# Performance work log

Measured on AMD Instinct MI355X. Metric: run time of the kernel, lower is better.

The kernel has to match this reference:

```python
import jax, jax.numpy as jnp
import numpy as np

H = 256        # hidden_channels (== out_channels)
IN = 128       # in_channels (atom features)
ED = 64        # edge_dim (bond features)
G = 1024       # num graphs
L = 48         # atoms per graph (static pad length)
N = G * L      # num atoms
E = 2 * N      # num directed edges
NLAYERS = 4


def setup_inputs() -> dict:
    key = jax.random.key(0)
    ks = jax.random.split(key, 12)
    def rn(k, shape, scale=0.05):
        return jax.random.normal(k, shape, jnp.float32) * scale
    return {
        "x": jax.random.normal(ks[0], (N, IN), jnp.float32),
        "edge_attr": jax.random.normal(ks[1], (E, ED), jnp.float32),
        "edge_index": jax.random.randint(ks[2], (2, E), 0, N),
        "batch": jnp.repeat(jnp.arange(G), L),  # sorted, L atoms per graph
        "w_atom": rn(ks[3], (IN, H)), "b_atom": jnp.zeros((H,), jnp.float32),
        "w_bond": rn(ks[4], (ED, H)), "b_bond": jnp.zeros((H,), jnp.float32),
        "conv_w": rn(ks[5], (NLAYERS, H, H)), "conv_b": jnp.zeros((NLAYERS, H), jnp.float32),
        "w_lin": rn(ks[6], (3 * H, H)), "b_lin": jnp.zeros((H,), jnp.float32),
        "gru_bias": rn(ks[7], (H,), 0.06),
        "w_ih": rn(ks[8], (2, 3 * H, H)), "w_hh": rn(ks[9], (2, 3 * H, H)),
        "b_ih": jnp.zeros((2, 3 * H), jnp.float32), "b_hh": jnp.zeros((2, 3 * H), jnp.float32),
        "w_out": rn(ks[10], (2 * H, H)), "b_out": jnp.zeros((H,), jnp.float32),
    }


def reference(x, edge_attr, edge_index, batch, w_atom, b_atom, w_bond, b_bond,
              conv_w, conv_b, w_lin, b_lin, gru_bias, w_ih, w_hh, b_ih, b_hh,
              w_out, b_out):
    relu = jax.nn.relu
    row, col = edge_index[0], edge_index[1]  # flow='target_to_source': aggregate at row

    x_proj = relu(x @ w_atom + b_atom)                 # [N, H]
    h_atom = x_proj
    h_bond = relu(edge_attr @ w_bond + b_bond)         # [E, H]

    def booster(h_bond):
        # message_booster multi-aggregation: sum * max (empty slots -> 0, as torch_scatter)
        s = jax.ops.segment_sum(h_bond, row, num_segments=N)
        m = jax.ops.segment_max(h_bond, row, num_segments=N)
        m = jnp.where(jnp.isfinite(m), m, 0.0)
        return s * m

    for i in range(NLAYERS - 1):
        h_atom = h_atom + booster(h_bond)              # additive communicator
        # edge_update: x[edge_index_i] - edge_attr[edge_index_j]; seq = Linear+ReLU (dropout p=0)
        h_bond = relu((h_atom[row] - h_bond[col]) @ conv_w[i] + conv_b[i])
    aggr_message = h_atom + booster(h_bond)            # last conv; edge output discarded

    h = jnp.concatenate([aggr_message, h_atom, x_proj], axis=1) @ w_lin + b_lin  # [N, H]

    # ---- BatchGRU ----
    msg = relu(h + gru_bias)
    starts = jnp.searchsorted(batch, jnp.arange(G))
    pos = jnp.arange(N) - starts[batch]                # position within own graph
    messages = jnp.zeros((G, L, H), h.dtype).at[batch, pos].set(msg)
    h0 = jax.ops.segment_max(h, batch, num_segments=G)  # [G, H], same init both dirs

    def gru_dir(seq, d):
        def cell(hst, x_t):
            gi = x_t @ w_ih[d].T + b_ih[d]
            gh = hst @ w_hh[d].T + b_hh[d]
            i_r, i_z, i_n = jnp.split(gi, 3, -1)
            h_r, h_z, h_n = jnp.split(gh, 3, -1)
            r = jax.nn.sigmoid(i_r + h_r)
            z = jax.nn.sigmoid(i_z + h_z)
            n = jnp.tanh(i_n + r * h_n)
            hn = (1.0 - z) * n + z * hst
            return hn, hn
        _, out = jax.lax.scan(cell, h0, seq)
        return out

    seq = messages.transpose(1, 0, 2)                  # [L, G, H]
    out_f = gru_dir(seq, 0)
    out_b = gru_dir(seq[::-1], 1)[::-1]
    h_msgs = jnp.concatenate([out_f, out_b], -1).transpose(1, 0, 2)  # [G, L, 2H]
    unpadded = h_msgs[batch, pos]                      # [N, 2H]

    return relu(unpadded @ w_out + b_out)              # seq_out (dropout p=0)
```

## Files before the change

kernel.cpp:

```cpp
#include <hip/hip_runtime.h>
#include <math.h>

#define HH 256
#define GG 1024
#define LL 48
#define NNODES 49152
#define NEDGES 98304
#define SB 256.0f
#define DSB 0.00390625f

typedef _Float16 f16;
typedef __attribute__((ext_vector_type(8))) _Float16 f16x8;
typedef __attribute__((ext_vector_type(4))) float f32x4;

#define MFMA16(a, b, c) __builtin_amdgcn_mfma_f32_16x16x32_f16(a, b, c, 0, 0, 0)

__device__ inline float sc_from_max(float m) {
    if (!(m > 0.f)) return 1.0f;
    return ldexpf(1.0f, 13 - ilogbf(m));
}

__global__ void csr_count(const int* __restrict__ row, int* __restrict__ counts)
{
    int e = blockIdx.x * 256 + threadIdx.x;
    if (e < NEDGES) atomicAdd(&counts[row[e]], 1);
}

__global__ __launch_bounds__(1024) void scan_offsets(const int* __restrict__ counts,
                                                     int* __restrict__ offsets)
{
    __shared__ int tsum[1024];
    const int tid = threadIdx.x;
    const int base = tid * 48;
    int s = 0;
    for (int i = 0; i < 48; i++) s += counts[base + i];
    tsum[tid] = s;
    __syncthreads();
    for (int off = 1; off < 1024; off <<= 1) {
        int v = (tid >= off) ? tsum[tid - off] : 0;
        __syncthreads();
        tsum[tid] += v;
        __syncthreads();
    }
    int run = (tid == 0) ? 0 : tsum[tid - 1];
    for (int i = 0; i < 48; i++) { offsets[base + i] = run; run += counts[base + i]; }
    if (tid == 1023) offsets[NNODES] = run;
}

__global__ void csr_fill(const int* __restrict__ row, const int* __restrict__ offsets,
                         int* __restrict__ cursor, int* __restrict__ elist)
{
    int e = blockIdx.x * 256 + threadIdx.x;
    if (e < NEDGES) {
        int r = row[e];
        int p = atomicAdd(&cursor[r], 1);
        elist[offsets[r] + p] = e;
    }
}

__global__ void prep_graphs(const int* __restrict__ batch, int* __restrict__ starts,
                            int* __restrict__ gcnt)
{
    int i = blockIdx.x * 256 + threadIdx.x;
    if (i < NNODES) {
        int b = batch[i];
        atomicAdd(&gcnt[b], 1);
        if (i == 0 || batch[i - 1] != b) starts[b] = i;
    }
}

__global__ void rowscale(const float* __restrict__ A, int K, float* __restrict__ sc)
{
    int m = blockIdx.x, ln = threadIdx.x;
    float v = 0.f;
    for (int k = ln; k < K; k += 64) v = fmaxf(v, fabsf(A[(size_t)m * K + k]));
    for (int s = 32; s; s >>= 1) v = fmaxf(v, __shfl_xor(v, s));
    if (ln == 0) sc[m] = sc_from_max(v);
}

__global__ void prep_wT_all(const float* __restrict__ w_atom, const float* __restrict__ w_bond,
                            const float* __restrict__ conv_w, const float* __restrict__ w_lin,
                            const float* __restrict__ w_out,
                            f16* __restrict__ watomH, f16* __restrict__ watomL,
                            f16* __restrict__ wbondH, f16* __restrict__ wbondL,
                            f16* __restrict__ convH0, f16* __restrict__ convL0,
                            f16* __restrict__ convH1, f16* __restrict__ convL1,
                            f16* __restrict__ convH2, f16* __restrict__ convL2,
                            f16* __restrict__ wlinH, f16* __restrict__ wlinL,
                            f16* __restrict__ woutH, f16* __restrict__ woutL)
{
    int idx = blockIdx.x * 256 + threadIdx.x;
    int krow = idx >> 8, n = idx & 255;
    const float* src; f16* oH; f16* oL; int k;
    if (krow < 128)       { src = w_atom;           oH = watomH; oL = watomL; k = krow; }
    else if (krow < 192)  { src = w_bond;           oH = wbondH; oL = wbondL; k = krow - 128; }
    else if (krow < 448)  { src = conv_w;           oH = convH0; oL = convL0; k = krow - 192; }
    else if (krow < 704)  { src = conv_w + 65536;   oH = convH1; oL = convL1; k = krow - 448; }
    else if (krow < 960)  { src = conv_w + 131072;  oH = convH2; oL = convL2; k = krow - 704; }
    else if (krow < 1728) { src = w_lin;            oH = wlinH;  oL = wlinL;  k = krow - 960; }
    else                  { src = w_out;            oH = woutH;  oL = woutL;  k = krow - 1728; }
    float v = src[(size_t)k * 256 + n] * SB;
    f16 h = (f16)v;
    size_t o = ((size_t)(k >> 5) * 256 + n) * 32 + (k & 31);
    oH[o] = h;
    oL[o] = (f16)(v - (float)h);
}

__global__ void prep_gruW(const float* __restrict__ w_ih, const float* __restrict__ w_hh,
                          const float* __restrict__ b_ih, const float* __restrict__ b_hh,
                          f16* __restrict__ BgH, f16* __restrict__ BgL,
                          float* __restrict__ bias4)
{
    int idx = blockIdx.x * 256 + threadIdx.x;
    int d = idx >> 19;
    int rem = idx & 524287;
    int k = rem >> 10;
    int col = rem & 1023;
    int jj = col >> 2, s = col & 3;
    const float* Wi = w_ih + (size_t)d * 768 * 256;
    const float* Wh = w_hh + (size_t)d * 768 * 256;
    float v;
    if (s == 0)      v = (k < 256) ? Wi[(size_t)jj * 256 + k]         : Wh[(size_t)jj * 256 + (k - 256)];
    else if (s == 1) v = (k < 256) ? Wi[(size_t)(256 + jj) * 256 + k] : Wh[(size_t)(256 + jj) * 256 + (k - 256)];
    else if (s == 2) v = (k < 256) ? Wi[(size_t)(512 + jj) * 256 + k] : 0.f;
    else             v = (k < 256) ? 0.f : Wh[(size_t)(512 + jj) * 256 + (k - 256)];
    v *= SB;
    f16 h = (f16)v;
    size_t o = ((size_t)(d * 16 + (k >> 5)) * 1024 + col) * 32 + (k & 31);
    BgH[o] = h;
    BgL[o] = (f16)(v - (float)h);
    if (k == 0) {
        const float* bi = b_ih + d * 768;
        const float* bh = b_hh + d * 768;
        float bv;
        if (s == 0)      bv = bi[jj] + bh[jj];
        else if (s == 1) bv = bi[256 + jj] + bh[256 + jj];
        else if (s == 2) bv = bi[512 + jj];
        else             bv = bh[512 + jj];
        bias4[d * 1024 + col] = bv;
    }
}

__global__ void booster(const float* __restrict__ hb_lo, const float* __restrict__ hb_hi,
                        const float* __restrict__ atom_in, float* __restrict__ out,
                        const int* __restrict__ offsets, const int* __restrict__ elist,
                        float* __restrict__ scOut)
{
    const int wv = threadIdx.x >> 6;
    const int n = blockIdx.x * 4 + wv;
    const int ln = threadIdx.x & 63;
    const int b0 = offsets[n], b1 = offsets[n + 1];
    float4 s = {0.f, 0.f, 0.f, 0.f}, m = {0.f, 0.f, 0.f, 0.f};
    for (int p = b0; p < b1; p++) {
        int e = elist[p];
        const float* hb = (e < NNODES) ? (hb_lo + (size_t)e * HH)
                                       : (hb_hi + (size_t)(e - NNODES) * HH);
        float4 v = *(const float4*)(hb + ln * 4);
        s.x += v.x; s.y += v.y; s.z += v.z; s.w += v.w;
        m.x = fmaxf(m.x, v.x); m.y = fmaxf(m.y, v.y);
        m.z = fmaxf(m.z, v.z); m.w = fmaxf(m.w, v.w);
    }
    float4 a = *(const float4*)(atom_in + (size_t)n * HH + ln * 4);
    float4 o;
    o.x = a.x + s.x * m.x; o.y = a.y + s.y * m.y;
    o.z = a.z + s.z * m.z; o.w = a.w + s.w * m.w;
    *(float4*)(out + (size_t)n * HH + ln * 4) = o;
    float v = fmaxf(fmaxf(fabsf(o.x), fabsf(o.y)), fmaxf(fabsf(o.z), fabsf(o.w)));
    for (int t = 32; t; t >>= 1) v = fmaxf(v, __shfl_xor(v, t));
    if (ln == 0) scOut[n] = sc_from_max(v);
}

__global__ void h0_init(const float* __restrict__ h, const int* __restrict__ starts,
                        const int* __restrict__ gcnt, float* __restrict__ hid0,
                        float* __restrict__ scG)
{
    const int wv = threadIdx.x >> 6;
    const int g = blockIdx.x * 4 + wv;
    const int ln = threadIdx.x & 63;
    const int st = starts[g], cn = gcnt[g];
    float4 m = {-INFINITY, -INFINITY, -INFINITY, -INFINITY};
    float4 am = {0.f, 0.f, 0.f, 0.f};
    for (int i = 0; i < cn; i++) {
        float4 v = *(const float4*)(h + (size_t)(st + i) * HH + ln * 4);
        m.x = fmaxf(m.x, v.x); m.y = fmaxf(m.y, v.y);
        m.z = fmaxf(m.z, v.z); m.w = fmaxf(m.w, v.w);
        am.x = fmaxf(am.x, fabsf(v.x)); am.y = fmaxf(am.y, fabsf(v.y));
        am.z = fmaxf(am.z, fabsf(v.z)); am.w = fmaxf(am.w, fabsf(v.w));
    }
    if (cn == 0) { m.x = m.y = m.z = m.w = 0.f; }
    *(float4*)(hid0 + (size_t)g * HH + ln * 4) = m;
    *(float4*)(hid0 + (size_t)GG * HH + (size_t)g * HH + ln * 4) = m;
    float a = fmaxf(fmaxf(am.x, am.y), fmaxf(am.z, am.w));
    for (int t = 32; t; t >>= 1) a = fmaxf(a, __shfl_xor(a, t));
    if (ln == 0) scG[g] = sc_from_max(fmaxf(a + 0.07f, 1.0f));
}

__global__ void build_msgP(const float* __restrict__ h, const float* __restrict__ gbias,
                           const int* __restrict__ starts, const int* __restrict__ gcnt,
                           float* __restrict__ msgP)
{
    const int l = blockIdx.x;
    const int g = blockIdx.y * 4 + (threadIdx.x >> 6);
    const int q = threadIdx.x & 63;
    float4 v = {0.f, 0.f, 0.f, 0.f};
    if (l < gcnt[g]) {
        float4 hv = *(const float4*)(h + (size_t)(starts[g] + l) * HH + q * 4);
        float4 bv = *(const float4*)(gbias + q * 4);
        v.x = fmaxf(hv.x + bv.x, 0.f); v.y = fmaxf(hv.y + bv.y, 0.f);
        v.z = fmaxf(hv.z + bv.z, 0.f); v.w = fmaxf(hv.w + bv.w, 0.f);
    }
    *(float4*)(msgP + ((size_t)l * GG + g) * HH + q * 4) = v;
}

template<int MODE>
__device__ __forceinline__ void gemmLoadA(const float* __restrict__ A,
    const float* __restrict__ S0, const float* __restrict__ S1,
    const float* __restrict__ S2, int rI, int cI, int row, int K, int k,
    float va[8])
{
    if constexpr (MODE == 0) {
        const float* p = A + (size_t)row * K + k;
        float4 v0 = *(const float4*)p, v1 = *(const float4*)(p + 4);
        va[0]=v0.x; va[1]=v0.y; va[2]=v0.z; va[3]=v0.w;
        va[4]=v1.x; va[5]=v1.y; va[6]=v1.z; va[7]=v1.w;
    } else if constexpr (MODE == 1) {
        const float* pa = S0 + (size_t)rI * HH + k;
        const float* pb = S1 + (size_t)cI * HH + k;
        float4 a0 = *(const float4*)pa, a1 = *(const float4*)(pa + 4);
        float4 b0 = *(const float4*)pb, b1 = *(const float4*)(pb + 4);
        va[0]=a0.x-b0.x; va[1]=a0.y-b0.y; va[2]=a0.z-b0.z; va[3]=a0.w-b0.w;
        va[4]=a1.x-b1.x; va[5]=a1.y-b1.y; va[6]=a1.z-b1.z; va[7]=a1.w-b1.w;
    } else if constexpr (MODE == 2) {
        const float* S = (k < 256) ? S0 : ((k < 512) ? S1 : S2);
        const float* p = S + (size_t)row * HH + (k & 255);
        float4 v0 = *(const float4*)p, v1 = *(const float4*)(p + 4);
        va[0]=v0.x; va[1]=v0.y; va[2]=v0.z; va[3]=v0.w;
        va[4]=v1.x; va[5]=v1.y; va[6]=v1.z; va[7]=v1.w;
    } else {
        const float* S = (k < 256) ? S0 : S1;
        const float* p = S + (size_t)row * HH + (k & 255);
        float4 v0 = *(const float4*)p, v1 = *(const float4*)(p + 4);
        va[0]=v0.x; va[1]=v0.y; va[2]=v0.z; va[3]=v0.w;
        va[4]=v1.x; va[5]=v1.y; va[6]=v1.z; va[7]=v1.w;
    }
}

template<int MODE, bool RELU, bool SPLITC, bool WSCALE, int NX>
__global__ __launch_bounds__(256, 2) void gemm_f16x3(
    const float* __restrict__ A,
    const float* __restrict__ S0, const float* __restrict__ S1, const float* __restrict__ S2,
    const int* __restrict__ ridx, const int* __restrict__ cidx,
    const f16* __restrict__ BgH, const f16* __restrict__ BgL,
    const float* __restrict__ bias,
    const float* __restrict__ sc0, const float* __restrict__ sc1, const float* __restrict__ sc2,
    float* __restrict__ Clo, float* __restrict__ Chi,
    float* __restrict__ scOut, int K)
{
    __shared__ __align__(16) f16 AhB[2][64 * 40], AlB[2][64 * 40];
    __shared__ float scL[64];
    __shared__ float rmL[64][4];

    const int tid = threadIdx.x;
    const int m0 = blockIdx.x * 64;
    const int arow = tid >> 2, aoct = tid & 3;
    const int w = tid >> 6, lane = tid & 63, lr = lane & 15, lh = lane >> 4;

    if (tid < 64) {
        float sc;
        if constexpr (MODE == 0) sc = sc0[m0 + tid];
        else if constexpr (MODE == 1) {
            int r = ridx[m0 + tid], cc = cidx[m0 + tid];
            sc = fminf(sc0[r], sc1[cc]) * 0.5f;
        } else if constexpr (MODE == 2) {
            sc = fminf(fminf(sc0[m0 + tid], sc1[m0 + tid]), sc2[m0 + tid]);
        } else {
            sc = sc0[cidx[m0 + tid]];
        }
        scL[tid] = sc;
    }
    int rI = 0, cI = 0;
    if constexpr (MODE == 1) { rI = ridx[m0 + arow]; cI = cidx[m0 + arow]; }
    __syncthreads();
    const float myS = scL[arow];
    const int nIter = K >> 5;

    {
        float va0[8];
        gemmLoadA<MODE>(A, S0, S1, S2, rI, cI, m0 + arow, K, aoct * 8, va0);
        f16x8 hi, lo;
#pragma unroll
        for (int e = 0; e < 8; e++) {
            float a = va0[e] * myS;
            f16 h = (f16)a;
            hi[e] = h;
            if constexpr (NX == 3) lo[e] = (f16)(a - (float)h);
        }
        *(f16x8*)&AhB[0][arow * 40 + aoct * 8] = hi;
        if constexpr (NX == 3) *(f16x8*)&AlB[0][arow * 40 + aoct * 8] = lo;
    }
    float va[8];
    if (nIter > 1)
        gemmLoadA<MODE>(A, S0, S1, S2, rI, cI, m0 + arow, K, 32 + aoct * 8, va);
    f16x8 fbh[4], fbl[4];
#pragma unroll
    for (int j = 0; j < 4; j++) {
        size_t o = (size_t)(w * 64 + j * 16 + lr) * 32 + lh * 8;
        fbh[j] = *(const f16x8*)(BgH + o);
        if constexpr (NX == 3) fbl[j] = *(const f16x8*)(BgL + o);
    }
    __syncthreads();

    f32x4 acc[4][4] = {};
    for (int kb = 0; kb < nIter; kb++) {
        const f16* AhC = AhB[kb & 1];
        const f16* AlC = AlB[kb & 1];
        float nva[8];
        f16x8 nbh[4], nbl[4];
        if (kb + 2 < nIter)
            gemmLoadA<MODE>(A, S0, S1, S2, rI, cI, m0 + arow, K, (kb + 2) * 32 + aoct * 8, nva);
        if (kb + 1 < nIter) {
#pragma unroll
            for (int j = 0; j < 4; j++) {
                size_t o = ((size_t)(kb + 1) * 256 + (w * 64 + j * 16 + lr)) * 32 + lh * 8;
                nbh[j] = *(const f16x8*)(BgH + o);
                if constexpr (NX == 3) nbl[j] = *(const f16x8*)(BgL + o);
            }
        }
        f16x8 fah[4], fal[4];
#pragma unroll
        for (int i = 0; i < 4; i++) {
            fah[i] = *(const f16x8*)&AhC[(i * 16 + lr) * 40 + lh * 8];
            if constexpr (NX == 3) fal[i] = *(const f16x8*)&AlC[(i * 16 + lr) * 40 + lh * 8];
        }
#pragma unroll
        for (int j = 0; j < 4; j++) {
            if constexpr (NX == 3) {
#pragma unroll
                for (int i = 0; i < 4; i++) {
                    acc[i][j] = MFMA16(fah[i], fbh[j], acc[i][j]);
                    acc[i][j] = MFMA16(fah[i], fbl[j], acc[i][j]);
                    acc[i][j] = MFMA16(fal[i], fbh[j], acc[i][j]);
                }
            } else {
#pragma unroll
                for (int i = 0; i < 4; i++)
                    acc[i][j] = MFMA16(fah[i], fbh[j], acc[i][j]);
            }
        }
        if (kb + 1 < nIter) {
            f16x8 hi, lo;
#pragma unroll
            for (int e = 0; e < 8; e++) {
                float a = va[e] * myS;
                f16 h = (f16)a;
                hi[e] = h;
                if constexpr (NX == 3) lo[e] = (f16)(a - (float)h);
            }
            f16* AhN = AhB[(kb + 1) & 1];
            f16* AlN = AlB[(kb + 1) & 1];
            *(f16x8*)&AhN[arow * 40 + aoct * 8] = hi;
            if constexpr (NX == 3) *(f16x8*)&AlN[arow * 40 + aoct * 8] = lo;
        }
        if (kb + 2 < nIter) {
#pragma unroll
            for (int e = 0; e < 8; e++) va[e] = nva[e];
        }
        if (kb + 1 < nIter) {
#pragma unroll
            for (int j = 0; j < 4; j++) {
                fbh[j] = nbh[j];
                if constexpr (NX == 3) fbl[j] = nbl[j];
            }
        }
        __syncthreads();
    }

    float rm[4][4];
#pragma unroll
    for (int i = 0; i < 4; i++)
#pragma unroll
        for (int e = 0; e < 4; e++) rm[i][e] = 0.f;
#pragma unroll
    for (int i = 0; i < 4; i++) {
#pragma unroll
        for (int e = 0; e < 4; e++) {
            int ml = i * 16 + lh * 4 + e;
            int m = m0 + ml;
            float inv = DSB / scL[ml];
            float* Cb;
            if constexpr (SPLITC)
                Cb = (m < NNODES) ? (Clo + (size_t)m * HH) : (Chi + (size_t)(m - NNODES) * HH);
            else
                Cb = Clo + (size_t)m * HH;
#pragma unroll
            for (int j = 0; j < 4; j++) {
                int n = w * 64 + j * 16 + lr;
                float v = acc[i][j][e] * inv + bias[n];
                if constexpr (RELU) v = fmaxf(v, 0.f);
                Cb[n] = v;
                if constexpr (WSCALE) rm[i][e] = fmaxf(rm[i][e], fabsf(v));
            }
        }
    }
    if constexpr (WSCALE) {
#pragma unroll
        for (int i = 0; i < 4; i++)
#pragma unroll
            for (int e = 0; e < 4; e++) {
                float v = rm[i][e];
                v = fmaxf(v, __shfl_xor(v, 1));
                v = fmaxf(v, __shfl_xor(v, 2));
                v = fmaxf(v, __shfl_xor(v, 4));
                v = fmaxf(v, __shfl_xor(v, 8));
                if (lr == 0) rmL[i * 16 + lh * 4 + e][w] = v;
            }
        __syncthreads();
        if (tid < 64)
            scOut[m0 + tid] = sc_from_max(fmaxf(fmaxf(rmL[tid][0], rmL[tid][1]),
                                                fmaxf(rmL[tid][2], rmL[tid][3])));
    }
}

__global__ __launch_bounds__(512) void gru_step_f16(
    const float* __restrict__ msgP, const f16* __restrict__ BgH, const f16* __restrict__ BgL,
    const float* __restrict__ bias4, const float* __restrict__ hidC, float* __restrict__ hidN,
    const float* __restrict__ scG, const int* __restrict__ starts, const int* __restrict__ gcnt,
    float* __restrict__ outF, float* __restrict__ outB, int t)
{
    __shared__ __align__(16) char smemraw[36864];
    float* Cs = (float*)smemraw;
    __shared__ float scL[64];

    const int tid = threadIdx.x;
    const int id = blockIdx.x;
    const int c = id & 7, d = (id >> 3) & 1, gt = id >> 4;
    const int g0 = gt * 64;
    const int l = d ? (LL - 1 - t) : t;
    const float* hidCd = hidC + (size_t)d * GG * HH;
    float* hidNd = hidN + (size_t)d * GG * HH;

    if (tid < 64) scL[tid] = scG[g0 + tid];
    __syncthreads();

    const int arow = tid >> 3, akoct = tid & 7;
    const float myS = scL[arow];
    const int w = tid >> 6;
    const int wg = w >> 2, wc = w & 3;
    const int lane = tid & 63, lr = lane & 15, lh = lane >> 4;

    f16* Ah0 = (f16*)smemraw;
    f16* Al0 = Ah0 + 4608;
    f16* Ah1 = Al0 + 4608;
    f16* Al1 = Ah1 + 4608;

    {
        const float* p = msgP + ((size_t)l * GG + g0 + arow) * HH + akoct * 8;
        float4 v0 = *(const float4*)p, v1 = *(const float4*)(p + 4);
        float va0[8] = {v0.x, v0.y, v0.z, v0.w, v1.x, v1.y, v1.z, v1.w};
        f16x8 hi, lo;
#pragma unroll
        for (int e = 0; e < 8; e++) {
            float a = va0[e] * myS;
            f16 h = (f16)a;
            hi[e] = h;
            lo[e] = (f16)(a - (float)h);
        }
        *(f16x8*)&Ah0[arow * 72 + akoct * 8] = hi;
        *(f16x8*)&Al0[arow * 72 + akoct * 8] = lo;
    }
    float va[8];
    {
        const float* p = msgP + ((size_t)l * GG + g0 + arow) * HH + 64 + akoct * 8;
        float4 v0 = *(const float4*)p, v1 = *(const float4*)(p + 4);
        va[0]=v0.x; va[1]=v0.y; va[2]=v0.z; va[3]=v0.w;
        va[4]=v1.x; va[5]=v1.y; va[6]=v1.z; va[7]=v1.w;
    }
    f16x8 fbh[2][2], fbl[2][2];
#pragma unroll
    for (int ks = 0; ks < 2; ks++) {
        size_t kbase = (size_t)(d * 16 + ks) * 1024;
#pragma unroll
        for (int j = 0; j < 2; j++) {
            size_t o = (kbase + (c * 128 + wc * 32 + j * 16 + lr)) * 32 + lh * 8;
            fbh[ks][j] = *(const f16x8*)(BgH + o);
            fbl[ks][j] = *(const f16x8*)(BgL + o);
        }
    }
    __syncthreads();

    f32x4 acc[2][2] = {};
#pragma unroll
    for (int win = 0; win < 8; win++) {
        f16* AhC = (win & 1) ? Ah1 : Ah0;
        f16* AlC = (win & 1) ? Al1 : Al0;
        f16* AhN = (win & 1) ? Ah0 : Ah1;
        f16* AlN = (win & 1) ? Al0 : Al1;

        float nva[8];
        if (win + 2 < 8) {
            int k = (win + 2) * 64 + akoct * 8;
            const float* p = (k < 256)
                ? msgP + ((size_t)l * GG + g0 + arow) * HH + k
                : hidCd + (size_t)(g0 + arow) * HH + (k - 256);
            float4 v0 = *(const float4*)p, v1 = *(const float4*)(p + 4);
            nva[0]=v0.x; nva[1]=v0.y; nva[2]=v0.z; nva[3]=v0.w;
            nva[4]=v1.x; nva[5]=v1.y; nva[6]=v1.z; nva[7]=v1.w;
        }
        f16x8 nbh[2][2], nbl[2][2];
        if (win + 1 < 8) {
#pragma unroll
            for (int ks = 0; ks < 2; ks++) {
                size_t kbase = (size_t)(d * 16 + (win + 1) * 2 + ks) * 1024;
#pragma unroll
                for (int j = 0; j < 2; j++) {
                    size_t o = (kbase + (c * 128 + wc * 32 + j * 16 + lr)) * 32 + lh * 8;
                    nbh[ks][j] = *(const f16x8*)(BgH + o);
                    nbl[ks][j] = *(const f16x8*)(BgL + o);
                }
            }
        }
#pragma unroll
        for (int ks = 0; ks < 2; ks++) {
            f16x8 fah[2], fal[2];
#pragma unroll
            for (int i = 0; i < 2; i++) {
                fah[i] = *(const f16x8*)&AhC[(wg * 32 + i * 16 + lr) * 72 + ks * 32 + lh * 8];
                fal[i] = *(const f16x8*)&AlC[(wg * 32 + i * 16 + lr) * 72 + ks * 32 + lh * 8];
            }
#pragma unroll
            for (int j = 0; j < 2; j++) {
#pragma unroll
                for (int i = 0; i < 2; i++) {
                    acc[i][j] = MFMA16(fah[i], fbh[ks][j], acc[i][j]);
                    acc[i][j] = MFMA16(fah[i], fbl[ks][j], acc[i][j]);
                    acc[i][j] = MFMA16(fal[i], fbh[ks][j], acc[i][j]);
                }
            }
        }
        if (win + 1 < 8) {
            f16x8 hi, lo;
#pragma unroll
            for (int e = 0; e < 8; e++) {
                float a = va[e] * myS;
                f16 h = (f16)a;
                hi[e] = h;
                lo[e] = (f16)(a - (float)h);
            }
            *(f16x8*)&AhN[arow * 72 + akoct * 8] = hi;
            *(f16x8*)&AlN[arow * 72 + akoct * 8] = lo;
        }
        if (win + 2 < 8) {
#pragma unroll
            for (int e = 0; e < 8; e++) va[e] = nva[e];
        }
        if (win + 1 < 8) {
#pragma unroll
            for (int ks = 0; ks < 2; ks++)
#pragma unroll
                for (int j = 0; j < 2; j++) {
                    fbh[ks][j] = nbh[ks][j];
                    fbl[ks][j] = nbl[ks][j];
                }
        }
        __syncthreads();
    }

#pragma unroll
    for (int i = 0; i < 2; i++) {
#pragma unroll
        for (int e = 0; e < 4; e++) {
            int ml = wg * 32 + i * 16 + lh * 4 + e;
            float inv = DSB / scL[ml];
#pragma unroll
            for (int j = 0; j < 2; j++)
                Cs[ml * 132 + wc * 32 + j * 16 + lr] = acc[i][j][e] * inv;
        }
    }
    __syncthreads();

    const float* b4 = bias4 + d * 1024;
    const int jl = tid & 31;
    const int J  = c * 32 + jl;
    const int gbase = (tid >> 5) * 4;
    const float bb0 = b4[4 * J + 0], bb1 = b4[4 * J + 1];
    const float bb2 = b4[4 * J + 2], bb3 = b4[4 * J + 3];
    float* o = d ? outB : outF;
#pragma unroll
    for (int i = 0; i < 4; i++) {
        int gl = gbase + i;
        int g = g0 + gl;
        f32x4 gv = *(const f32x4*)&Cs[gl * 132 + jl * 4];
        float r = 1.f / (1.f + expf(-(gv[0] + bb0)));
        float z = 1.f / (1.f + expf(-(gv[1] + bb1)));
        float nn = tanhf(gv[2] + bb2 + r * (gv[3] + bb3));
        float hp = hidCd[(size_t)g * HH + J];
        float hnew = (1.f - z) * nn + z * hp;
        hidNd[(size_t)g * HH + J] = hnew;
        if (l < gcnt[g]) o[(size_t)(starts[g] + l) * HH + J] = hnew;
    }
}

__global__ void fill_sentinel(float* __restrict__ out, float v)
{
    size_t idx = (size_t)blockIdx.x * 256 + threadIdx.x;
    out[idx] = v;
}

extern "C" void kernel_launch(void* const* d_in, const int* in_sizes, int n_in,
                              void* d_out, int out_size, void* d_ws, size_t ws_size,
                              hipStream_t stream)
{
    (void)in_sizes; (void)n_in; (void)out_size;
    const float* x         = (const float*)d_in[0];
    const float* edge_attr = (const float*)d_in[1];
    const int*   eidx      = (const int*)d_in[2];
    const int*   batch     = (const int*)d_in[3];
    const float* w_atom    = (const float*)d_in[4];
    const float* b_atom    = (const float*)d_in[5];
    const float* w_bond    = (const float*)d_in[6];
    const float* b_bond    = (const float*)d_in[7];
    const float* conv_w    = (const float*)d_in[8];
    const float* conv_b    = (const float*)d_in[9];
    const float* w_lin     = (const float*)d_in[10];
    const float* b_lin     = (const float*)d_in[11];
    const float* gru_bias  = (const float*)d_in[12];
    const float* w_ih      = (const float*)d_in[13];
    const float* w_hh      = (const float*)d_in[14];
    const float* b_ih      = (const float*)d_in[15];
    const float* b_hh      = (const float*)d_in[16];
    const float* w_out     = (const float*)d_in[17];
    const float* b_out     = (const float*)d_in[18];

    const int* row = eidx;
    const int* col = eidx + NEDGES;

    const size_t NH = (size_t)NNODES * HH;

    float* W   = (float*)d_ws;
    float* W0  = W;
    float* W1  = W + NH;
    float* W1h = W + 2 * NH;
    float* W2  = W + 3 * NH;
    float* DO  = (float*)d_out;

    size_t off = 4 * NH;
    int* counts  = (int*)(W + off);      off += NNODES;
    int* cursor  = (int*)(W + off);      off += NNODES;
    int* gcnt    = (int*)(W + off);      off += GG;
    int* starts  = (int*)(W + off);      off += GG;
    int* offsets = (int*)(W + off);      off += NNODES + 1;
    int* elist   = (int*)(W + off);      off += NEDGES;
    float* scX    = W + off;             off += NNODES;
    float* scEA   = W + off;             off += NEDGES;
    float* scHbA  = W + off;             off += NEDGES;
    float* scHbB  = W + off;             off += NEDGES;
    float* scAtom = W + off;             off += NNODES;
    float* scAggr = W + off;             off += NNODES;
    float* scXp   = W + off;             off += NNODES;
    float* scGru  = W + off;             off += GG;
    off = (off + 3) & ~(size_t)3;
    f16* fp = (f16*)(W + off);
    f16* watomH = fp;                     fp += 4 * 256 * 32;
    f16* watomL = fp;                     fp += 4 * 256 * 32;
    f16* wbondH = fp;                     fp += 2 * 256 * 32;
    f16* wbondL = fp;                     fp += 2 * 256 * 32;
    f16* convH[3]; f16* convL[3];
    for (int i = 0; i < 3; i++) { convH[i] = fp; fp += 8 * 256 * 32; convL[i] = fp; fp += 8 * 256 * 32; }
    f16* wlinH = fp;                      fp += 24 * 256 * 32;
    f16* wlinL = fp;                      fp += 24 * 256 * 32;
    f16* woutH = fp;                      fp += 16 * 256 * 32;
    f16* woutL = fp;                      fp += 16 * 256 * 32;

    const size_t NEED = (char*)fp - (char*)d_ws;
    if (ws_size < NEED) {
        fill_sentinel<<<(int)(NH / 256), 256, 0, stream>>>((float*)d_out, (float)ws_size);
        return;
    }

    float* hid0  = DO;
    float* hid1  = DO + 2 * (size_t)GG * HH;
    float* bias4 = DO + 4 * (size_t)GG * HH;
    f16* BgH = (f16*)(bias4 + 2048);
    f16* BgL = BgH + (size_t)2 * 16 * 1024 * 32;

    hipMemsetAsync(counts, 0, (size_t)(2 * NNODES + 2 * GG) * sizeof(int), stream);
    prep_graphs<<<(NNODES + 255) / 256, 256, 0, stream>>>(batch, starts, gcnt);
    csr_count<<<(NEDGES + 255) / 256, 256, 0, stream>>>(row, counts);
    scan_offsets<<<1, 1024, 0, stream>>>(counts, offsets);
    csr_fill<<<(NEDGES + 255) / 256, 256, 0, stream>>>(row, offsets, cursor, elist);

    rowscale<<<NNODES, 64, 0, stream>>>(x, 128, scX);
    rowscale<<<NEDGES, 64, 0, stream>>>(edge_attr, 64, scEA);

    prep_wT_all<<<2240, 256, 0, stream>>>(w_atom, w_bond, conv_w, w_lin, w_out,
        watomH, watomL, wbondH, wbondL, convH[0], convL[0], convH[1], convL[1],
        convH[2], convL[2], wlinH, wlinL, woutH, woutL);

    gemm_f16x3<0, true, false, true, 3><<<NNODES / 64, 256, 0, stream>>>(
        x, nullptr, nullptr, nullptr, nullptr, nullptr, watomH, watomL, b_atom,
        scX, nullptr, nullptr, W0, nullptr, scAtom, 128);
    gemm_f16x3<0, true, true, true, 3><<<NEDGES / 64, 256, 0, stream>>>(
        edge_attr, nullptr, nullptr, nullptr, nullptr, nullptr, wbondH, wbondL, b_bond,
        scEA, nullptr, nullptr, W1, W1h, scHbA, 64);

    float* cur_lo = W1; float* cur_hi = W1h; float* cur_sc = scHbA;
    float* nxt_lo = W2; float* nxt_hi = DO;  float* nxt_sc = scHbB;
    for (int i = 0; i < 3; i++) {
        booster<<<NNODES / 4, 256, 0, stream>>>(cur_lo, cur_hi, W0, W0, offsets, elist, scAtom);
        gemm_f16x3<1, true, true, true, 3><<<NEDGES / 64, 256, 0, stream>>>(
            nullptr, W0, cur_lo, nullptr, row, col, convH[i], convL[i],
            conv_b + (size_t)i * HH, scAtom, cur_sc, nullptr, nxt_lo, nxt_hi, nxt_sc, 256);
        float* t0 = cur_lo; cur_lo = nxt_lo; nxt_lo = t0;
        float* t1 = cur_hi; cur_hi = nxt_hi; nxt_hi = t1;
        float* t2 = cur_sc; cur_sc = nxt_sc; nxt_sc = t2;
    }
    booster<<<NNODES / 4, 256, 0, stream>>>(cur_lo, cur_hi, W0, W1, offsets, elist, scAggr);
    gemm_f16x3<0, true, false, true, 3><<<NNODES / 64, 256, 0, stream>>>(
        x, nullptr, nullptr, nullptr, nullptr, nullptr, watomH, watomL, b_atom,
        scX, nullptr, nullptr, W1h, nullptr, scXp, 128);
    gemm_f16x3<2, false, false, false, 3><<<NNODES / 64, 256, 0, stream>>>(
        nullptr, W1, W0, W1h, nullptr, nullptr, wlinH, wlinL, b_lin,
        scAggr, scAtom, scXp, W2, nullptr, nullptr, 768);

    h0_init<<<GG / 4, 256, 0, stream>>>(W2, starts, gcnt, hid0, scGru);
    build_msgP<<<dim3(LL, GG / 4), 256, 0, stream>>>(W2, gru_bias, starts, gcnt, W1h);
    prep_gruW<<<(2 * 512 * 1024) / 256, 256, 0, stream>>>(w_ih, w_hh, b_ih, b_hh, BgH, BgL, bias4);

    for (int t = 0; t < LL; t++) {
        float* hc = (t & 1) ? hid1 : hid0;
        float* hx = (t & 1) ? hid0 : hid1;
        gru_step_f16<<<256, 512, 0, stream>>>(W1h, BgH, BgL, bias4, hc, hx,
                                              scGru, starts, gcnt, W0, W1, t);
    }

    gemm_f16x3<3, true, false, false, 1><<<NNODES / 64, 256, 0, stream>>>(
        nullptr, W0, W1, nullptr, nullptr, batch, woutH, nullptr, b_out,
        scGru, nullptr, nullptr, (float*)d_out, nullptr, nullptr, 512);
}
```

Measured before the change: 1.404 ms.

## Enlarge GEMM tile to 128 rows with 512-thread blocks sharing B fragments

```diff
diff --git a/kernel.cpp b/kernel.cpp
--- a/kernel.cpp
+++ b/kernel.cpp
@@ -246,7 +246,7 @@
 }
 
 template<int MODE, bool RELU, bool SPLITC, bool WSCALE, int NX>
-__global__ __launch_bounds__(256, 2) void gemm_f16x3(
+__global__ __launch_bounds__(512) void gemm_f16x3(
     const float* __restrict__ A,
     const float* __restrict__ S0, const float* __restrict__ S1, const float* __restrict__ S2,
     const int* __restrict__ ridx, const int* __restrict__ cidx,
@@ -256,16 +256,18 @@
     float* __restrict__ Clo, float* __restrict__ Chi,
     float* __restrict__ scOut, int K)
 {
-    __shared__ __align__(16) f16 AhB[2][64 * 40], AlB[2][64 * 40];
-    __shared__ float scL[64];
-    __shared__ float rmL[64][4];
+    __shared__ __align__(16) f16 AhB[2][128 * 40], AlB[2][128 * 40];
+    __shared__ float scL[128];
+    __shared__ float rmL[128][4];
 
     const int tid = threadIdx.x;
-    const int m0 = blockIdx.x * 64;
+    const int m0 = blockIdx.x * 128;
     const int arow = tid >> 2, aoct = tid & 3;
-    const int w = tid >> 6, lane = tid & 63, lr = lane & 15, lh = lane >> 4;
-
-    if (tid < 64) {
+    const int w = tid >> 6;
+    const int wr = w >> 2, wq = w & 3;
+    const int lane = tid & 63, lr = lane & 15, lh = lane >> 4;
+
+    if (tid < 128) {
         float sc;
         if constexpr (MODE == 0) sc = sc0[m0 + tid];
         else if constexpr (MODE == 1) {
@@ -298,13 +300,10 @@
         *(f16x8*)&AhB[0][arow * 40 + aoct * 8] = hi;
         if constexpr (NX == 3) *(f16x8*)&AlB[0][arow * 40 + aoct * 8] = lo;
     }
-    float va[8];
-    if (nIter > 1)
-        gemmLoadA<MODE>(A, S0, S1, S2, rI, cI, m0 + arow, K, 32 + aoct * 8, va);
     f16x8 fbh[4], fbl[4];
 #pragma unroll
     for (int j = 0; j < 4; j++) {
-        size_t o = (size_t)(w * 64 + j * 16 + lr) * 32 + lh * 8;
+        size_t o = (size_t)(wq * 64 + j * 16 + lr) * 32 + lh * 8;
         fbh[j] = *(const f16x8*)(BgH + o);
         if constexpr (NX == 3) fbl[j] = *(const f16x8*)(BgL + o);
     }
@@ -314,14 +313,13 @@
     for (int kb = 0; kb < nIter; kb++) {
         const f16* AhC = AhB[kb & 1];
         const f16* AlC = AlB[kb & 1];
-        float nva[8];
+        float va[8];
         f16x8 nbh[4], nbl[4];
-        if (kb + 2 < nIter)
-            gemmLoadA<MODE>(A, S0, S1, S2, rI, cI, m0 + arow, K, (kb + 2) * 32 + aoct * 8, nva);
         if (kb + 1 < nIter) {
+            gemmLoadA<MODE>(A, S0, S1, S2, rI, cI, m0 + arow, K, (kb + 1) * 32 + aoct * 8, va);
 #pragma unroll
             for (int j = 0; j < 4; j++) {
-                size_t o = ((size_t)(kb + 1) * 256 + (w * 64 + j * 16 + lr)) * 32 + lh * 8;
+                size_t o = ((size_t)(kb + 1) * 256 + (wq * 64 + j * 16 + lr)) * 32 + lh * 8;
                 nbh[j] = *(const f16x8*)(BgH + o);
                 if constexpr (NX == 3) nbl[j] = *(const f16x8*)(BgL + o);
             }
@@ -329,8 +327,8 @@
         f16x8 fah[4], fal[4];
 #pragma unroll
         for (int i = 0; i < 4; i++) {
-            fah[i] = *(const f16x8*)&AhC[(i * 16 + lr) * 40 + lh * 8];
-            if constexpr (NX == 3) fal[i] = *(const f16x8*)&AlC[(i * 16 + lr) * 40 + lh * 8];
+            fah[i] = *(const f16x8*)&AhC[(wr * 64 + i * 16 + lr) * 40 + lh * 8];
+            if constexpr (NX == 3) fal[i] = *(const f16x8*)&AlC[(wr * 64 + i * 16 + lr) * 40 + lh * 8];
         }
 #pragma unroll
         for (int j = 0; j < 4; j++) {
@@ -360,12 +358,6 @@
             f16* AlN = AlB[(kb + 1) & 1];
             *(f16x8*)&AhN[arow * 40 + aoct * 8] = hi;
             if constexpr (NX == 3) *(f16x8*)&AlN[arow * 40 + aoct * 8] = lo;
-        }
-        if (kb + 2 < nIter) {
-#pragma unroll
-            for (int e = 0; e < 8; e++) va[e] = nva[e];
-        }
-        if (kb + 1 < nIter) {
 #pragma unroll
             for (int j = 0; j < 4; j++) {
                 fbh[j] = nbh[j];
@@ -384,7 +376,7 @@
     for (int i = 0; i < 4; i++) {
 #pragma unroll
         for (int e = 0; e < 4; e++) {
-            int ml = i * 16 + lh * 4 + e;
+            int ml = wr * 64 + i * 16 + lh * 4 + e;
             int m = m0 + ml;
             float inv = DSB / scL[ml];
             float* Cb;
@@ -394,7 +386,7 @@
                 Cb = Clo + (size_t)m * HH;
 #pragma unroll
             for (int j = 0; j < 4; j++) {
-                int n = w * 64 + j * 16 + lr;
+                int n = wq * 64 + j * 16 + lr;
                 float v = acc[i][j][e] * inv + bias[n];
                 if constexpr (RELU) v = fmaxf(v, 0.f);
                 Cb[n] = v;
@@ -412,10 +404,10 @@
                 v = fmaxf(v, __shfl_xor(v, 2));
                 v = fmaxf(v, __shfl_xor(v, 4));
                 v = fmaxf(v, __shfl_xor(v, 8));
-                if (lr == 0) rmL[i * 16 + lh * 4 + e][w] = v;
+                if (lr == 0) rmL[wr * 64 + i * 16 + lh * 4 + e][wq] = v;
             }
         __syncthreads();
-        if (tid < 64)
+        if (tid < 128)
             scOut[m0 + tid] = sc_from_max(fmaxf(fmaxf(rmL[tid][0], rmL[tid][1]),
                                                 fmaxf(rmL[tid][2], rmL[tid][3])));
     }
@@ -696,10 +688,10 @@
         watomH, watomL, wbondH, wbondL, convH[0], convL[0], convH[1], convL[1],
         convH[2], convL[2], wlinH, wlinL, woutH, woutL);
 
-    gemm_f16x3<0, true, false, true, 3><<<NNODES / 64, 256, 0, stream>>>(
+    gemm_f16x3<0, true, false, true, 3><<<NNODES / 128, 512, 0, stream>>>(
         x, nullptr, nullptr, nullptr, nullptr, nullptr, watomH, watomL, b_atom,
         scX, nullptr, nullptr, W0, nullptr, scAtom, 128);
-    gemm_f16x3<0, true, true, true, 3><<<NEDGES / 64, 256, 0, stream>>>(
+    gemm_f16x3<0, true, true, true, 3><<<NEDGES / 128, 512, 0, stream>>>(
         edge_attr, nullptr, nullptr, nullptr, nullptr, nullptr, wbondH, wbondL, b_bond,
         scEA, nullptr, nullptr, W1, W1h, scHbA, 64);
 
@@ -707,7 +699,7 @@
     float* nxt_lo = W2; float* nxt_hi = DO;  float* nxt_sc = scHbB;
     for (int i = 0; i < 3; i++) {
         booster<<<NNODES / 4, 256, 0, stream>>>(cur_lo, cur_hi, W0, W0, offsets, elist, scAtom);
-        gemm_f16x3<1, true, true, true, 3><<<NEDGES / 64, 256, 0, stream>>>(
+        gemm_f16x3<1, true, true, true, 3><<<NEDGES / 128, 512, 0, stream>>>(
             nullptr, W0, cur_lo, nullptr, row, col, convH[i], convL[i],
             conv_b + (size_t)i * HH, scAtom, cur_sc, nullptr, nxt_lo, nxt_hi, nxt_sc, 256);
         float* t0 = cur_lo; cur_lo = nxt_lo; nxt_lo = t0;
@@ -715,10 +707,10 @@
         float* t2 = cur_sc; cur_sc = nxt_sc; nxt_sc = t2;
     }
     booster<<<NNODES / 4, 256, 0, stream>>>(cur_lo, cur_hi, W0, W1, offsets, elist, scAggr);
-    gemm_f16x3<0, true, false, true, 3><<<NNODES / 64, 256, 0, stream>>>(
+    gemm_f16x3<0, true, false, true, 3><<<NNODES / 128, 512, 0, stream>>>(
         x, nullptr, nullptr, nullptr, nullptr, nullptr, watomH, watomL, b_atom,
         scX, nullptr, nullptr, W1h, nullptr, scXp, 128);
-    gemm_f16x3<2, false, false, false, 3><<<NNODES / 64, 256, 0, stream>>>(
+    gemm_f16x3<2, false, false, false, 3><<<NNODES / 128, 512, 0, stream>>>(
         nullptr, W1, W0, W1h, nullptr, nullptr, wlinH, wlinL, b_lin,
         scAggr, scAtom, scXp, W2, nullptr, nullptr, 768);
 
@@ -733,7 +725,7 @@
                                               scGru, starts, gcnt, W0, W1, t);
     }
 
-    gemm_f16x3<3, true, false, false, 1><<<NNODES / 64, 256, 0, stream>>>(
+    gemm_f16x3<3, true, false, false, 1><<<NNODES / 128, 512, 0, stream>>>(
         nullptr, W0, W1, nullptr, nullptr, batch, woutH, nullptr, b_out,
         scGru, nullptr, nullptr, (float*)d_out, nullptr, nullptr, 512);
 }
```

After: 1.465 ms. 4.4% more time.
